# Optimization experiments

Hardware: AMD Instinct MI355X
Metric: run time of the kernel (lower is better)

The kernel has to match this reference:

```python
import jax, jax.numpy as jnp
import numpy as np

B, S, HID = 2, 2048, 1024
H, D = 16, HID // 16  # heads, head_dim
ROPE_BASE = 10000.0


def setup_inputs() -> dict:
    key = jax.random.key(0)
    k1, k2, k3, k4 = jax.random.split(key, 4)
    scale = 1.0 / np.sqrt(HID)
    return {
        "hidden_states": jax.random.normal(k1, (B, S, HID), dtype=jnp.float32),
        "attention_mask": jnp.zeros((B, 1, 1, S), dtype=jnp.float32),
        "Wq": jax.random.normal(k2, (HID, HID), dtype=jnp.float32) * scale,
        "Wk": jax.random.normal(k3, (HID, HID), dtype=jnp.float32) * scale,
        "Wv": jax.random.normal(k4, (HID, HID), dtype=jnp.float32) * scale,
    }


def _rope_cos_sin(seq_len, dim, dtype):
    inv_freq = 1.0 / (ROPE_BASE ** (jnp.arange(0, dim, 2, dtype=jnp.float32) / dim))
    freqs = jnp.arange(seq_len, dtype=jnp.float32)[:, None] * inv_freq[None, :]  # (S, D/2)
    emb = jnp.concatenate([freqs, freqs], axis=-1)  # (S, D)
    return jnp.cos(emb).astype(dtype), jnp.sin(emb).astype(dtype)


def _rotate_half(x):
    x1, x2 = jnp.split(x, 2, axis=-1)
    return jnp.concatenate([-x2, x1], axis=-1)


def reference(hidden_states, attention_mask, Wq, Wk, Wv):
    b, s, _ = hidden_states.shape
    # QKV projections (no bias), split into heads: (b, H, s, D)
    def proj(W):
        return jnp.einsum('bse,de->bsd', hidden_states, W).reshape(b, s, H, D).transpose(0, 2, 1, 3)
    q, k, v = proj(Wq), proj(Wk), proj(Wv)
    # Rotary embedding on q, k over sequence positions
    cos, sin = _rope_cos_sin(s, D, hidden_states.dtype)  # (s, D)
    cos = cos[None, None]  # (1,1,s,D)
    sin = sin[None, None]
    q = q * cos + _rotate_half(q) * sin
    k = k * cos + _rotate_half(k) * sin
    # Scaled dot-product attention with additive mask
    scores = jnp.einsum('bhqd,bhkd->bhqk', q, k) / jnp.sqrt(jnp.asarray(D, hidden_states.dtype))
    scores = scores + attention_mask
    probs = jax.nn.softmax(scores, axis=-1)  # dropout p=0 (eval) -> identity
    ctx = jnp.einsum('bhqk,bhkd->bhqd', probs, v)
    return ctx.transpose(0, 2, 1, 3).reshape(b, s, H * D)
```

## Files before the change

kernel.cpp:

```cpp
#include <hip/hip_runtime.h>
#include <stdint.h>

typedef unsigned short u16;
typedef short bf16x8 __attribute__((ext_vector_type(8)));
typedef float f32x4 __attribute__((ext_vector_type(4)));

#define S_ 2048
#define HID_ 1024
#define H_ 16
#define D_ 64

#define LOG2E 1.4426950408889634f
#define SCALE_LOG2 0.18033688011112042f
#define MAXC_LOG2 11.541560327111707f

__device__ __forceinline__ u16 f2bf(float f) {
  uint32_t x = __builtin_bit_cast(uint32_t, f);
  uint32_t r = (x + 0x7fffu + ((x >> 16) & 1u)) >> 16;
  return (u16)r;
}
__device__ __forceinline__ uint32_t packbf2(float a, float b) {
  return (uint32_t)f2bf(a) | ((uint32_t)f2bf(b) << 16);
}
__device__ __forceinline__ uint32_t permpack(float a, float b) {
  return __builtin_amdgcn_perm(__builtin_bit_cast(uint32_t, b),
                               __builtin_bit_cast(uint32_t, a), 0x07060302u);
}

__device__ __forceinline__ void gl2lds16(const void* g, void* l) {
  __builtin_amdgcn_global_load_lds(
      (const __attribute__((address_space(1))) unsigned int*)g,
      (__attribute__((address_space(3))) unsigned int*)l, 16, 0, 0);
}

#define NX_ (1 << 20)
#define NW_ (1 << 18)
#define NROPE_ 65536
__global__ void prep_kernel(const float* __restrict__ X, const float* __restrict__ Wq,
                            const float* __restrict__ Wk, const float* __restrict__ Wv,
                            const float* __restrict__ mask, u16* __restrict__ Xb,
                            u16* __restrict__ Wqb, u16* __restrict__ Wkb,
                            u16* __restrict__ Wvb, float* __restrict__ cos_t,
                            float* __restrict__ sin_t, float* __restrict__ mask2) {
  int i = blockIdx.x * 256 + threadIdx.x;
  if (i < NX_ + 3 * NW_) {
    const float* src;
    u16* dst;
    int off;
    if (i < NX_) {
      src = X; dst = Xb; off = i;
    } else if (i < NX_ + NW_) {
      src = Wq; dst = Wqb; off = i - NX_;
    } else if (i < NX_ + 2 * NW_) {
      src = Wk; dst = Wkb; off = i - NX_ - NW_;
    } else {
      src = Wv; dst = Wvb; off = i - NX_ - 2 * NW_;
    }
    float4 v = ((const float4*)src)[off];
    uint2 packed;
    packed.x = packbf2(v.x, v.y);
    packed.y = packbf2(v.z, v.w);
    ((uint2*)dst)[off] = packed;
  } else if (i < NX_ + 3 * NW_ + NROPE_) {
    int t = i - (NX_ + 3 * NW_);
    int s = t >> 5, j = t & 31;
    float invf = powf(10000.0f, -(float)j * (1.0f / 32.0f));
    float ang = (float)s * invf;
    cos_t[t] = cosf(ang);
    sin_t[t] = sinf(ang);
  } else {
    int t = i - (NX_ + 3 * NW_ + NROPE_);
    mask2[t] = fmaf(mask[t], LOG2E, -MAXC_LOG2);
  }
}

__global__ __launch_bounds__(256) void qkv_gemm_kernel(
    const u16* __restrict__ X, const u16* __restrict__ Wq, const u16* __restrict__ Wk,
    const u16* __restrict__ Wv, const float* __restrict__ cos_t,
    const float* __restrict__ sin_t, u16* __restrict__ Q, u16* __restrict__ K,
    u16* __restrict__ Vt) {
  __shared__ char smem[65536];
  int tid = threadIdx.x;
  int lane = tid & 63, wave = tid >> 6;
  int wm = wave >> 1, wn = wave & 1;
  int quad = lane >> 4, l16 = lane & 15;
  int which = blockIdx.x >> 3;
  int nbase = (blockIdx.x & 7) * 128;
  int mbase = blockIdx.y * 128;
  const u16* W = (which == 0) ? Wq : (which == 1) ? Wk : Wv;

#pragma unroll
  for (int it = 0; it < 4; ++it) {
    int i = it * 256 + tid;
    int r = i >> 3, gs = i & 7, gsrc = gs ^ (r & 7);
    gl2lds16(X + (size_t)(mbase + r) * HID_ + gsrc * 8, smem + i * 16);
    gl2lds16(W + (size_t)(nbase + r) * HID_ + gsrc * 8, smem + 32768 + i * 16);
  }

  f32x4 acc[4][4] = {};

  for (int kk = 0; kk < 16; ++kk) {
    char* As = smem + (kk & 1) * 16384;
    char* Bs = smem + 32768 + (kk & 1) * 16384;
    __syncthreads();

    if (kk < 15) {
      int k0n = (kk + 1) * 64;
      char* An = smem + ((kk + 1) & 1) * 16384;
      char* Bn = smem + 32768 + ((kk + 1) & 1) * 16384;
#pragma unroll
      for (int it = 0; it < 4; ++it) {
        int i = it * 256 + tid;
        int r = i >> 3, gs = i & 7, gsrc = gs ^ (r & 7);
        gl2lds16(X + (size_t)(mbase + r) * HID_ + k0n + gsrc * 8, An + i * 16);
        gl2lds16(W + (size_t)(nbase + r) * HID_ + k0n + gsrc * 8, Bn + i * 16);
      }
    }

#pragma unroll
    for (int kh = 0; kh < 2; ++kh) {
      bf16x8 afrag[4], bfrag[4];
#pragma unroll
      for (int i4 = 0; i4 < 4; ++i4) {
        int r = wm * 64 + i4 * 16 + l16;
        int L = r * 8 + ((kh * 4 + quad) ^ (r & 7));
        afrag[i4] = *(const bf16x8*)(As + L * 16);
      }
#pragma unroll
      for (int j4 = 0; j4 < 4; ++j4) {
        int r = wn * 64 + j4 * 16 + l16;
        int L = r * 8 + ((kh * 4 + quad) ^ (r & 7));
        bfrag[j4] = *(const bf16x8*)(Bs + L * 16);
      }
      if (which == 2) {
#pragma unroll
        for (int i4 = 0; i4 < 4; ++i4)
#pragma unroll
          for (int j4 = 0; j4 < 4; ++j4)
            acc[i4][j4] = __builtin_amdgcn_mfma_f32_16x16x32_bf16(afrag[i4], bfrag[j4],
                                                                  acc[i4][j4], 0, 0, 0);
      } else {
#pragma unroll
        for (int i4 = 0; i4 < 4; ++i4)
#pragma unroll
          for (int j4 = 0; j4 < 4; ++j4)
            acc[i4][j4] = __builtin_amdgcn_mfma_f32_16x16x32_bf16(bfrag[j4], afrag[i4],
                                                                  acc[i4][j4], 0, 0, 0);
      }
    }
  }

  if (which == 2) {
#pragma unroll
    for (int i4 = 0; i4 < 4; ++i4)
#pragma unroll
      for (int j4 = 0; j4 < 4; ++j4) {
        int m = mbase + wm * 64 + i4 * 16 + quad * 4;
        int n = nbase + wn * 64 + j4 * 16 + l16;
        int b = m >> 11, s0 = m & 2047;
        int h = n >> 6, d = n & 63;
        uint2 pk;
        pk.x = packbf2(acc[i4][j4][0], acc[i4][j4][1]);
        pk.y = packbf2(acc[i4][j4][2], acc[i4][j4][3]);
        *(uint2*)(Vt + (((size_t)(b * H_ + h)) * D_ + d) * S_ + s0) = pk;
      }
  } else {
    u16* dst = (which == 0) ? Q : K;
#pragma unroll
    for (int i4 = 0; i4 < 4; ++i4)
#pragma unroll
      for (int j4 = 0; j4 < 2; ++j4) {
        int m = mbase + wm * 64 + i4 * 16 + l16;
        int n1 = nbase + wn * 64 + j4 * 16 + quad * 4;
        int b = m >> 11, s = m & 2047;
        int h = n1 >> 6, d1 = n1 & 63;
        float4 c4 = *(const float4*)(cos_t + s * 32 + d1);
        float4 s4 = *(const float4*)(sin_t + s * 32 + d1);
        float y1[4], y2[4];
#pragma unroll
        for (int r = 0; r < 4; ++r) {
          float cr = ((const float*)&c4)[r], sr = ((const float*)&s4)[r];
          float x1 = acc[i4][j4][r], x2 = acc[i4][j4 + 2][r];
          y1[r] = x1 * cr - x2 * sr;
          y2[r] = x2 * cr + x1 * sr;
        }
        size_t base = ((size_t)(b * H_ + h) * S_ + s) * D_;
        uint2 p1, p2;
        p1.x = packbf2(y1[0], y1[1]);
        p1.y = packbf2(y1[2], y1[3]);
        p2.x = packbf2(y2[0], y2[1]);
        p2.y = packbf2(y2[2], y2[3]);
        *(uint2*)(dst + base + d1) = p1;
        *(uint2*)(dst + base + d1 + 32) = p2;
      }
  }
}

__device__ __forceinline__ void pv_step(const char* Pw, const char* Vp, int quad, int l16,
                                        const bf16x8& ones, f32x4 (*o)[4], f32x4* lacc) {
  bf16x8 p[2][2];
#pragma unroll
  for (int qb = 0; qb < 2; ++qb) {
    const char* Pr = Pw + qb * 2048;
#pragma unroll
    for (int kh = 0; kh < 2; ++kh) {
      int c0 = kh * 8 + quad * 2;
      union { uint2 u[2]; bf16x8 v; } cv;
      cv.u[0] = *(const uint2*)(Pr + l16 * 128 + ((c0) ^ l16) * 8);
      cv.u[1] = *(const uint2*)(Pr + l16 * 128 + ((c0 + 1) ^ l16) * 8);
      p[qb][kh] = cv.v;
    }
    lacc[qb] = __builtin_amdgcn_mfma_f32_16x16x32_bf16(p[qb][0], ones, lacc[qb], 0, 0, 0);
    lacc[qb] = __builtin_amdgcn_mfma_f32_16x16x32_bf16(p[qb][1], ones, lacc[qb], 0, 0, 0);
  }
#pragma unroll
  for (int jd = 0; jd < 4; ++jd) {
    int r = jd * 16 + l16;
#pragma unroll
    for (int kh = 0; kh < 2; ++kh) {
      int L = r * 8 + ((kh * 4 + quad) ^ (r & 7));
      bf16x8 vf = *(const bf16x8*)(Vp + L * 16);
      o[0][jd] = __builtin_amdgcn_mfma_f32_16x16x32_bf16(p[0][kh], vf, o[0][jd], 0, 0, 0);
      o[1][jd] = __builtin_amdgcn_mfma_f32_16x16x32_bf16(p[1][kh], vf, o[1][jd], 0, 0, 0);
    }
  }
}

__global__ __launch_bounds__(256, 2) void flash_kernel(
    const u16* __restrict__ Q, const u16* __restrict__ K, const u16* __restrict__ Vt,
    const float* __restrict__ mask2, float* __restrict__ out) {
  __shared__ char smem[65536];
  int tid = threadIdx.x, wave = tid >> 6;
  int lane = tid & 63;
  int quad = lane >> 4, l16 = lane & 15;
  int bh = blockIdx.y, b = bh >> 4, h = bh & 15;
  int qbase = blockIdx.x * 128;
  int qw = qbase + wave * 32;
  char* Pw = smem + 49152 + wave * 4096;
  const float* m2row = mask2 + b * S_;
  const u16* Kbase = K + (size_t)bh * S_ * D_;
  const u16* Vbase = Vt + (size_t)bh * D_ * S_;

  bf16x8 qfrag[2][2];
#pragma unroll
  for (int qb = 0; qb < 2; ++qb) {
    const u16* qp = Q + ((size_t)bh * S_ + qw + qb * 16 + l16) * D_ + quad * 8;
    qfrag[qb][0] = *(const bf16x8*)qp;
    qfrag[qb][1] = *(const bf16x8*)(qp + 32);
  }
  bf16x8 ones;
#pragma unroll
  for (int j = 0; j < 8; ++j) ones[j] = (short)0x3f80;

  f32x4 o[2][4] = {};
  f32x4 lacc[2] = {};

#pragma unroll
  for (int half = 0; half < 2; ++half) {
    int i = half * 256 + tid;
    int r = i >> 3, gs = i & 7, gsrc = gs ^ (r & 7);
    gl2lds16(Kbase + (size_t)r * D_ + gsrc * 8, smem + i * 16);
    gl2lds16(Vbase + (size_t)r * S_ + gsrc * 8, smem + 8192 + i * 16);
  }
  float4 mv[4];
#pragma unroll
  for (int jt = 0; jt < 4; ++jt) mv[jt] = *(const float4*)(m2row + jt * 16 + quad * 4);

  for (int kt = 0; kt < 32; ++kt) {
    char* Ks = smem + (kt % 3) * 16384;
    __syncthreads();

    if (kt < 31) {
      char* Kn = smem + ((kt + 1) % 3) * 16384;
      char* Vn = Kn + 8192;
      int nb = (kt + 1) * 64;
#pragma unroll
      for (int half = 0; half < 2; ++half) {
        int i = half * 256 + tid;
        int r = i >> 3, gs = i & 7, gsrc = gs ^ (r & 7);
        gl2lds16(Kbase + (size_t)(nb + r) * D_ + gsrc * 8, Kn + i * 16);
        gl2lds16(Vbase + (size_t)r * S_ + nb + gsrc * 8, Vn + i * 16);
      }
    }

    if (kt > 0) {
      const char* Vp = smem + ((kt - 1) % 3) * 16384 + 8192;
      pv_step(Pw, Vp, quad, l16, ones, o, lacc);
    }

    f32x4 s[2][4] = {};
#pragma unroll
    for (int jt = 0; jt < 4; ++jt) {
      int r = jt * 16 + l16;
#pragma unroll
      for (int kh = 0; kh < 2; ++kh) {
        int L = r * 8 + ((kh * 4 + quad) ^ (r & 7));
        bf16x8 kf = *(const bf16x8*)(Ks + L * 16);
        s[0][jt] = __builtin_amdgcn_mfma_f32_16x16x32_bf16(kf, qfrag[0][kh], s[0][jt], 0, 0, 0);
        s[1][jt] = __builtin_amdgcn_mfma_f32_16x16x32_bf16(kf, qfrag[1][kh], s[1][jt], 0, 0, 0);
      }
    }

#pragma unroll
    for (int qb = 0; qb < 2; ++qb)
#pragma unroll
      for (int jt = 0; jt < 4; ++jt) {
        float pf[4];
#pragma unroll
        for (int r = 0; r < 4; ++r) {
          float mvr = ((const float*)&mv[jt])[r];
          pf[r] = __builtin_amdgcn_exp2f(fmaf(s[qb][jt][r], SCALE_LOG2, mvr));
        }
        uint2 pk;
        pk.x = permpack(pf[0], pf[1]);
        pk.y = permpack(pf[2], pf[3]);
        int chunk = (jt * 4 + quad) ^ l16;
        *(uint2*)(Pw + qb * 2048 + l16 * 128 + chunk * 8) = pk;
      }

    if (kt < 31) {
#pragma unroll
      for (int jt = 0; jt < 4; ++jt)
        mv[jt] = *(const float4*)(m2row + (kt + 1) * 64 + jt * 16 + quad * 4);
    }
  }

  pv_step(Pw, smem + 16384 + 8192, quad, l16, ones, o, lacc);

  float inv[2][4];
#pragma unroll
  for (int qb = 0; qb < 2; ++qb)
#pragma unroll
    for (int r = 0; r < 4; ++r) inv[qb][r] = 1.0f / lacc[qb][r];
#pragma unroll
  for (int qb = 0; qb < 2; ++qb)
#pragma unroll
    for (int jd = 0; jd < 4; ++jd) {
#pragma unroll
      for (int r = 0; r < 4; ++r) {
        int d = jd * 16 + l16;
        int q = qw + qb * 16 + quad * 4 + r;
        out[(((size_t)b * S_ + q) * H_ + h) * D_ + d] = o[qb][jd][r] * inv[qb][r];
      }
    }
}

extern "C" void kernel_launch(void* const* d_in, const int* in_sizes, int n_in,
                              void* d_out, int out_size, void* d_ws, size_t ws_size,
                              hipStream_t stream) {
  const float* hid = (const float*)d_in[0];
  const float* mask = (const float*)d_in[1];
  const float* Wq = (const float*)d_in[2];
  const float* Wk = (const float*)d_in[3];
  const float* Wv = (const float*)d_in[4];
  float* out = (float*)d_out;
  char* ws = (char*)d_ws;

  u16* Xbf = (u16*)ws;
  u16* Wqb = (u16*)(ws + (8u << 20));
  u16* Wkb = (u16*)(ws + (10u << 20));
  u16* Wvb = (u16*)(ws + (12u << 20));
  u16* Qb = (u16*)(ws + (14u << 20));
  u16* Kb = (u16*)(ws + (22u << 20));
  u16* Vtb = (u16*)(ws + (30u << 20));
  float* cos_t = (float*)(ws + (38u << 20));
  float* sin_t = (float*)(ws + (38u << 20) + (256u << 10));
  float* mask2 = (float*)(ws + (38u << 20) + (512u << 10));

  prep_kernel<<<7440, 256, 0, stream>>>(hid, Wq, Wk, Wv, mask, Xbf, Wqb, Wkb, Wvb,
                                        cos_t, sin_t, mask2);
  qkv_gemm_kernel<<<dim3(24, 32), 256, 0, stream>>>(Xbf, Wqb, Wkb, Wvb, cos_t, sin_t,
                                                    Qb, Kb, Vtb);
  flash_kernel<<<dim3(16, 32), 256, 0, stream>>>(Qb, Kb, Vtb, mask2, out);
}
```

Measured before the change: 170.1 us.

## Single-buffer QKV GEMM for occupancy and peel flash loop with MFMA priority hints

The QKV GEMM drops LDS double buffering: it uses one 32KB buffer with a load after compute and a second barrier, and asks for 3 blocks per CU through launch bounds so more blocks can hide latency. The flash kernel peels its first and last iterations, removing the per-iteration branches, and wraps the MFMA sections in s_setprio so waves doing matrix work are scheduled ahead of others. The GEMM change serialises loads and compute inside a block, and relies on the extra occupancy to cover that.

```diff
diff --git a/kernel.cpp b/kernel.cpp
--- a/kernel.cpp
+++ b/kernel.cpp
@@ -74,12 +74,12 @@
   }
 }
 
-__global__ __launch_bounds__(256) void qkv_gemm_kernel(
+__global__ __launch_bounds__(256, 3) void qkv_gemm_kernel(
     const u16* __restrict__ X, const u16* __restrict__ Wq, const u16* __restrict__ Wk,
     const u16* __restrict__ Wv, const float* __restrict__ cos_t,
     const float* __restrict__ sin_t, u16* __restrict__ Q, u16* __restrict__ K,
     u16* __restrict__ Vt) {
-  __shared__ char smem[65536];
+  __shared__ char smem[32768];
   int tid = threadIdx.x;
   int lane = tid & 63, wave = tid >> 6;
   int wm = wave >> 1, wn = wave & 1;
@@ -94,28 +94,15 @@
     int i = it * 256 + tid;
     int r = i >> 3, gs = i & 7, gsrc = gs ^ (r & 7);
     gl2lds16(X + (size_t)(mbase + r) * HID_ + gsrc * 8, smem + i * 16);
-    gl2lds16(W + (size_t)(nbase + r) * HID_ + gsrc * 8, smem + 32768 + i * 16);
+    gl2lds16(W + (size_t)(nbase + r) * HID_ + gsrc * 8, smem + 16384 + i * 16);
   }
 
   f32x4 acc[4][4] = {};
 
   for (int kk = 0; kk < 16; ++kk) {
-    char* As = smem + (kk & 1) * 16384;
-    char* Bs = smem + 32768 + (kk & 1) * 16384;
-    __syncthreads();
-
-    if (kk < 15) {
-      int k0n = (kk + 1) * 64;
-      char* An = smem + ((kk + 1) & 1) * 16384;
-      char* Bn = smem + 32768 + ((kk + 1) & 1) * 16384;
-#pragma unroll
-      for (int it = 0; it < 4; ++it) {
-        int i = it * 256 + tid;
-        int r = i >> 3, gs = i & 7, gsrc = gs ^ (r & 7);
-        gl2lds16(X + (size_t)(mbase + r) * HID_ + k0n + gsrc * 8, An + i * 16);
-        gl2lds16(W + (size_t)(nbase + r) * HID_ + k0n + gsrc * 8, Bn + i * 16);
-      }
-    }
+    __syncthreads();
+    const char* As = smem;
+    const char* Bs = smem + 16384;
 
 #pragma unroll
     for (int kh = 0; kh < 2; ++kh) {
@@ -146,6 +133,18 @@
           for (int j4 = 0; j4 < 4; ++j4)
             acc[i4][j4] = __builtin_amdgcn_mfma_f32_16x16x32_bf16(bfrag[j4], afrag[i4],
                                                                   acc[i4][j4], 0, 0, 0);
+      }
+    }
+
+    __syncthreads();
+    if (kk < 15) {
+      int k0n = (kk + 1) * 64;
+#pragma unroll
+      for (int it = 0; it < 4; ++it) {
+        int i = it * 256 + tid;
+        int r = i >> 3, gs = i & 7, gsrc = gs ^ (r & 7);
+        gl2lds16(X + (size_t)(mbase + r) * HID_ + k0n + gsrc * 8, smem + i * 16);
+        gl2lds16(W + (size_t)(nbase + r) * HID_ + k0n + gsrc * 8, smem + 16384 + i * 16);
       }
     }
   }
@@ -226,6 +225,52 @@
   }
 }
 
+__device__ __forceinline__ void qk_step(const char* Ks, const bf16x8 (*qfrag)[2], int quad,
+                                        int l16, f32x4 (*s)[4]) {
+#pragma unroll
+  for (int jt = 0; jt < 4; ++jt) {
+    int r = jt * 16 + l16;
+#pragma unroll
+    for (int kh = 0; kh < 2; ++kh) {
+      int L = r * 8 + ((kh * 4 + quad) ^ (r & 7));
+      bf16x8 kf = *(const bf16x8*)(Ks + L * 16);
+      s[0][jt] = __builtin_amdgcn_mfma_f32_16x16x32_bf16(kf, qfrag[0][kh], s[0][jt], 0, 0, 0);
+      s[1][jt] = __builtin_amdgcn_mfma_f32_16x16x32_bf16(kf, qfrag[1][kh], s[1][jt], 0, 0, 0);
+    }
+  }
+}
+
+__device__ __forceinline__ void softmax_store(const f32x4 (*s)[4], const float4* mv,
+                                              char* Pw, int quad, int l16) {
+#pragma unroll
+  for (int qb = 0; qb < 2; ++qb)
+#pragma unroll
+    for (int jt = 0; jt < 4; ++jt) {
+      float pf[4];
+#pragma unroll
+      for (int r = 0; r < 4; ++r) {
+        float mvr = ((const float*)&mv[jt])[r];
+        pf[r] = __builtin_amdgcn_exp2f(fmaf(s[qb][jt][r], SCALE_LOG2, mvr));
+      }
+      uint2 pk;
+      pk.x = permpack(pf[0], pf[1]);
+      pk.y = permpack(pf[2], pf[3]);
+      int chunk = (jt * 4 + quad) ^ l16;
+      *(uint2*)(Pw + qb * 2048 + l16 * 128 + chunk * 8) = pk;
+    }
+}
+
+__device__ __forceinline__ void stage_kv(const u16* Kbase, const u16* Vbase, char* Kn,
+                                         int nb, int tid) {
+#pragma unroll
+  for (int half = 0; half < 2; ++half) {
+    int i = half * 256 + tid;
+    int r = i >> 3, gs = i & 7, gsrc = gs ^ (r & 7);
+    gl2lds16(Kbase + (size_t)(nb + r) * D_ + gsrc * 8, Kn + i * 16);
+    gl2lds16(Vbase + (size_t)r * S_ + nb + gsrc * 8, Kn + 8192 + i * 16);
+  }
+}
+
 __global__ __launch_bounds__(256, 2) void flash_kernel(
     const u16* __restrict__ Q, const u16* __restrict__ K, const u16* __restrict__ Vt,
     const float* __restrict__ mask2, float* __restrict__ out) {
@@ -255,74 +300,51 @@
   f32x4 o[2][4] = {};
   f32x4 lacc[2] = {};
 
-#pragma unroll
-  for (int half = 0; half < 2; ++half) {
-    int i = half * 256 + tid;
-    int r = i >> 3, gs = i & 7, gsrc = gs ^ (r & 7);
-    gl2lds16(Kbase + (size_t)r * D_ + gsrc * 8, smem + i * 16);
-    gl2lds16(Vbase + (size_t)r * S_ + gsrc * 8, smem + 8192 + i * 16);
-  }
+  stage_kv(Kbase, Vbase, smem, 0, tid);
   float4 mv[4];
 #pragma unroll
   for (int jt = 0; jt < 4; ++jt) mv[jt] = *(const float4*)(m2row + jt * 16 + quad * 4);
 
-  for (int kt = 0; kt < 32; ++kt) {
+  {
+    __syncthreads();
+    stage_kv(Kbase, Vbase, smem + 16384, 64, tid);
+    f32x4 s[2][4] = {};
+    __builtin_amdgcn_s_setprio(1);
+    qk_step(smem, qfrag, quad, l16, s);
+    __builtin_amdgcn_s_setprio(0);
+    softmax_store(s, mv, Pw, quad, l16);
+#pragma unroll
+    for (int jt = 0; jt < 4; ++jt)
+      mv[jt] = *(const float4*)(m2row + 64 + jt * 16 + quad * 4);
+  }
+
+  for (int kt = 1; kt <= 30; ++kt) {
     char* Ks = smem + (kt % 3) * 16384;
     __syncthreads();
-
-    if (kt < 31) {
-      char* Kn = smem + ((kt + 1) % 3) * 16384;
-      char* Vn = Kn + 8192;
-      int nb = (kt + 1) * 64;
-#pragma unroll
-      for (int half = 0; half < 2; ++half) {
-        int i = half * 256 + tid;
-        int r = i >> 3, gs = i & 7, gsrc = gs ^ (r & 7);
-        gl2lds16(Kbase + (size_t)(nb + r) * D_ + gsrc * 8, Kn + i * 16);
-        gl2lds16(Vbase + (size_t)r * S_ + nb + gsrc * 8, Vn + i * 16);
-      }
-    }
-
-    if (kt > 0) {
-      const char* Vp = smem + ((kt - 1) % 3) * 16384 + 8192;
-      pv_step(Pw, Vp, quad, l16, ones, o, lacc);
-    }
+    stage_kv(Kbase, Vbase, smem + ((kt + 1) % 3) * 16384, (kt + 1) * 64, tid);
+
+    __builtin_amdgcn_s_setprio(1);
+    const char* Vp = smem + ((kt - 1) % 3) * 16384 + 8192;
+    pv_step(Pw, Vp, quad, l16, ones, o, lacc);
 
     f32x4 s[2][4] = {};
-#pragma unroll
-    for (int jt = 0; jt < 4; ++jt) {
-      int r = jt * 16 + l16;
-#pragma unroll
-      for (int kh = 0; kh < 2; ++kh) {
-        int L = r * 8 + ((kh * 4 + quad) ^ (r & 7));
-        bf16x8 kf = *(const bf16x8*)(Ks + L * 16);
-        s[0][jt] = __builtin_amdgcn_mfma_f32_16x16x32_bf16(kf, qfrag[0][kh], s[0][jt], 0, 0, 0);
-        s[1][jt] = __builtin_amdgcn_mfma_f32_16x16x32_bf16(kf, qfrag[1][kh], s[1][jt], 0, 0, 0);
-      }
-    }
-
-#pragma unroll
-    for (int qb = 0; qb < 2; ++qb)
-#pragma unroll
-      for (int jt = 0; jt < 4; ++jt) {
-        float pf[4];
-#pragma unroll
-        for (int r = 0; r < 4; ++r) {
-          float mvr = ((const float*)&mv[jt])[r];
-          pf[r] = __builtin_amdgcn_exp2f(fmaf(s[qb][jt][r], SCALE_LOG2, mvr));
-        }
-        uint2 pk;
-        pk.x = permpack(pf[0], pf[1]);
-        pk.y = permpack(pf[2], pf[3]);
-        int chunk = (jt * 4 + quad) ^ l16;
-        *(uint2*)(Pw + qb * 2048 + l16 * 128 + chunk * 8) = pk;
-      }
-
-    if (kt < 31) {
-#pragma unroll
-      for (int jt = 0; jt < 4; ++jt)
-        mv[jt] = *(const float4*)(m2row + (kt + 1) * 64 + jt * 16 + quad * 4);
-    }
+    qk_step(Ks, qfrag, quad, l16, s);
+    __builtin_amdgcn_s_setprio(0);
+
+    softmax_store(s, mv, Pw, quad, l16);
+#pragma unroll
+    for (int jt = 0; jt < 4; ++jt)
+      mv[jt] = *(const float4*)(m2row + (kt + 1) * 64 + jt * 16 + quad * 4);
+  }
+
+  {
+    __syncthreads();
+    __builtin_amdgcn_s_setprio(1);
+    pv_step(Pw, smem + 0 * 16384 + 8192, quad, l16, ones, o, lacc);
+    f32x4 s[2][4] = {};
+    qk_step(smem + 16384, qfrag, quad, l16, s);
+    __builtin_amdgcn_s_setprio(0);
+    softmax_store(s, mv, Pw, quad, l16);
   }
 
   pv_step(Pw, smem + 16384 + 8192, quad, l16, ones, o, lacc);
```

Measured after the change: 197.1 us. +15.9%, slower.
